# Kernel tuning notes

Measured on AMD Instinct MI355X. Metric: run time of the kernel, lower is better.

## Reference

```python
import jax, jax.numpy as jnp
import numpy as np

T, B, H, N = 1024, 8, 8, 32  # x dim D = H*N*N = 8192


def setup_inputs() -> dict:
    key = jax.random.key(0)
    x = jax.random.normal(key, (T, B, H * N * N), dtype=jnp.float32)
    S = jnp.zeros((B, H, N, N), dtype=jnp.float32)
    scale = jnp.float32(1.0)  # init_scale
    bias = jnp.float32(2.0)   # init_bias
    return {"x": x, "S": S, "scale": scale, "bias": bias}


def reference(x, S, scale, bias):
    Tt, Bb, D = x.shape
    _, Hh, n, _ = S.shape
    xr = x.reshape(Tt, Bb, Hh, n, n)  # [T,B,H,n,n]

    def step(S_c, A):
        # A: [B,H,n,n]
        k = A.mean(axis=-1)            # mean over dim 2 per head -> [B,H,n]
        v = A.mean(axis=-2)            # mean over dim 1 per head -> [B,H,n]
        A_mean = A.mean(axis=(-1, -2))  # [B,H]
        beta = jax.nn.sigmoid(scale * A_mean + bias)  # [B,H]
        k_norm = k / (jnp.linalg.norm(k, axis=-1, keepdims=True) + 1e-6)
        retrieved = jnp.einsum('bhij,bhj->bhi', S_c, k_norm)
        delta = v - retrieved
        outer = delta[..., :, None] * k_norm[..., None, :]  # [B,H,n,n]
        S_new = jnp.tanh(beta[..., None, None] * S_c + outer)
        Sq = jnp.einsum('bhij,bhj->bhi', S_new, k_norm)     # [B,H,n]
        out = Sq * jax.nn.silu(Sq)                          # [B,H,n]
        return S_new, out.reshape(Bb, Hh * n)

    S_final, output = jax.lax.scan(step, S, xr)  # output: [T,B,H*n]
    return output, S_final
```

## Files before the change

kernel.cpp:

```cpp
#include <hip/hip_runtime.h>
#include <math.h>

#define T_STEPS 1024
#define NBH     64
#define NTILE   65536
#define NCHAIN  2048
#define UNROLL  8

static __device__ __forceinline__ float fast_rcp(float x) {
  return __builtin_amdgcn_rcpf(x);
}
static __device__ __forceinline__ float fast_sigmoid(float x) {
  return fast_rcp(1.0f + __expf(-x));
}
static __device__ __forceinline__ float fast_tanh(float x) {
  return 1.0f - 2.0f * fast_rcp(1.0f + __expf(2.0f * x));
}

template <int CTRL>
static __device__ __forceinline__ float dpp_add(float x) {
  int y = __builtin_amdgcn_update_dpp(0, __float_as_int(x), CTRL, 0xF, 0xF, true);
  return x + __int_as_float(y);
}

static __device__ __forceinline__ float red32(float x) {
  x = dpp_add<0xB1>(x);
  x = dpp_add<0x4E>(x);
  x = dpp_add<0x141>(x);
  x = dpp_add<0x140>(x);
  int y = __builtin_amdgcn_ds_swizzle(__float_as_int(x), 0x401F);
  return x + __int_as_float(y);
}

__global__ __launch_bounds__(256) void stats_kernel(
    const float* __restrict__ x, const float* __restrict__ scale_p,
    const float* __restrict__ bias_p, float* __restrict__ knT,
    float* __restrict__ vvT, float* __restrict__ bbT) {
  const int tid = threadIdx.x;
  const int l   = tid & 63;
  const int m   = l & 7;
  const int g   = l >> 3;
  const int wid    = (blockIdx.x * blockDim.x + tid) >> 6;
  const int nwaves = (gridDim.x * blockDim.x) >> 6;
  const float sc = scale_p[0], bi = bias_p[0];

  for (int tile = wid; tile < NTILE; tile += nwaves) {
    const int t  = tile >> 6;
    const int bh = tile & 63;
    const float4* xp = (const float4*)(x + (size_t)tile * 1024);
    const float4 a0 = xp[l];
    const float4 a1 = xp[l + 64];
    const float4 a2 = xp[l + 128];
    const float4 a3 = xp[l + 192];

    float r0 = (a0.x + a0.y) + (a0.z + a0.w);
    float r1 = (a1.x + a1.y) + (a1.z + a1.w);
    float r2 = (a2.x + a2.y) + (a2.z + a2.w);
    float r3 = (a3.x + a3.y) + (a3.z + a3.w);
    r0 += __shfl_xor(r0, 1); r1 += __shfl_xor(r1, 1);
    r2 += __shfl_xor(r2, 1); r3 += __shfl_xor(r3, 1);
    r0 += __shfl_xor(r0, 2); r1 += __shfl_xor(r1, 2);
    r2 += __shfl_xor(r2, 2); r3 += __shfl_xor(r3, 2);
    r0 += __shfl_xor(r0, 4); r1 += __shfl_xor(r1, 4);
    r2 += __shfl_xor(r2, 4); r3 += __shfl_xor(r3, 4);

    float c0 = a0.x + a1.x + a2.x + a3.x;
    float c1 = a0.y + a1.y + a2.y + a3.y;
    float c2 = a0.z + a1.z + a2.z + a3.z;
    float c3 = a0.w + a1.w + a2.w + a3.w;
    c0 += __shfl_xor(c0, 8);  c1 += __shfl_xor(c1, 8);
    c2 += __shfl_xor(c2, 8);  c3 += __shfl_xor(c3, 8);
    c0 += __shfl_xor(c0, 16); c1 += __shfl_xor(c1, 16);
    c2 += __shfl_xor(c2, 16); c3 += __shfl_xor(c3, 16);
    c0 += __shfl_xor(c0, 32); c1 += __shfl_xor(c1, 32);
    c2 += __shfl_xor(c2, 32); c3 += __shfl_xor(c3, 32);

    float t1 = (r0 + r1) + (r2 + r3);
    float t2 = (r0 * r0 + r1 * r1) + (r2 * r2 + r3 * r3);
    t1 += __shfl_xor(t1, 8);  t2 += __shfl_xor(t2, 8);
    t1 += __shfl_xor(t1, 16); t2 += __shfl_xor(t2, 16);
    t1 += __shfl_xor(t1, 32); t2 += __shfl_xor(t2, 32);
    const float sumk  = t1 * (1.0f / 32.0f);
    const float norm  = sqrtf(t2) * (1.0f / 32.0f);
    const float ks    = (1.0f / 32.0f) * fast_rcp(norm + 1e-6f);

    const size_t rec = ((size_t)bh * T_STEPS + t) * 32;
    if (m == 0) {
      float* kp = knT + rec + g;
      kp[0]  = r0 * ks;
      kp[8]  = r1 * ks;
      kp[16] = r2 * ks;
      kp[24] = r3 * ks;
    }
    if (l < 8) {
      float4 vq;
      vq.x = c0 * (1.0f / 32.0f); vq.y = c1 * (1.0f / 32.0f);
      vq.z = c2 * (1.0f / 32.0f); vq.w = c3 * (1.0f / 32.0f);
      ((float4*)(vvT + rec))[m] = vq;
    }
    if (l == 0) {
      const float mean = sumk * (1.0f / 32.0f);
      bbT[(size_t)bh * T_STEPS + t] = fast_sigmoid(sc * mean + bi);
    }
  }
}

__global__ __launch_bounds__(256) void scan_kernel(
    const float* __restrict__ S0, const float* __restrict__ knT,
    const float* __restrict__ vvT, const float* __restrict__ bbT,
    float* __restrict__ out, float* __restrict__ Sfin) {
  const int tid   = threadIdx.x;
  const int chain = blockIdx.x * 8 + (tid >> 5);
  const int j     = tid & 31;
  const int bh    = chain >> 5;
  const int i     = chain & 31;

  float S = S0[(size_t)bh * 1024 + i * 32 + j];

  const float* knp = knT + (size_t)bh * T_STEPS * 32 + j;
  const float* vvp = vvT + (size_t)bh * T_STEPS * 32 + i;
  const float* bbp = bbT + (size_t)bh * T_STEPS;

  float rkn[UNROLL], rv[UNROLL], rb[UNROLL];
#pragma unroll
  for (int u = 0; u < UNROLL; ++u) {
    rkn[u] = knp[u * 32];
    rv[u]  = vvp[u * 32];
    rb[u]  = bbp[u];
  }

  float* outp = out + chain;

  for (int t0 = 0; t0 < T_STEPS; t0 += UNROLL) {
    float nkn[UNROLL], nv[UNROLL], nb[UNROLL];
#pragma unroll
    for (int u = 0; u < UNROLL; ++u) {
      int tn = t0 + UNROLL + u;
      tn = tn < T_STEPS ? tn : (T_STEPS - 1);
      nkn[u] = knp[(size_t)tn * 32];
      nv[u]  = vvp[(size_t)tn * 32];
      nb[u]  = bbp[tn];
    }
#pragma unroll
    for (int u = 0; u < UNROLL; ++u) {
      const float knc = rkn[u], vc = rv[u], bc = rb[u];
      const float r = red32(S * knc);
      S = fast_tanh(bc * S + (vc - r) * knc);
      const float q  = red32(S * knc);
      const float o  = q * q * fast_sigmoid(q);
      if (j == 0) outp[(size_t)(t0 + u) * 2048] = o;
    }
#pragma unroll
    for (int u = 0; u < UNROLL; ++u) {
      rkn[u] = nkn[u]; rv[u] = nv[u]; rb[u] = nb[u];
    }
  }

  Sfin[(size_t)bh * 1024 + i * 32 + j] = S;
}

extern "C" void kernel_launch(void* const* d_in, const int* in_sizes, int n_in,
                              void* d_out, int out_size, void* d_ws, size_t ws_size,
                              hipStream_t stream) {
  const float* x     = (const float*)d_in[0];
  const float* S0    = (const float*)d_in[1];
  const float* scale = (const float*)d_in[2];
  const float* bias  = (const float*)d_in[3];
  float* out = (float*)d_out;

  float* knT = (float*)d_ws;
  float* vvT = knT + (size_t)NTILE * 32;
  float* bbT = vvT + (size_t)NTILE * 32;

  stats_kernel<<<2048, 256, 0, stream>>>(x, scale, bias, knT, vvT, bbT);

  float* Sfin = out + (size_t)T_STEPS * 2048;
  scan_kernel<<<NCHAIN / 8, 256, 0, stream>>>(S0, knT, vvT, bbT, out, Sfin);
}
```

Before: 568.5 us.

## Pack two state columns per lane, transpose stats to time-major, batch output stores

The stats kernel now writes k_norm and v in a [bh][dim][T] layout, so the scan can load 16 consecutive timesteps with float4 loads and double-buffer them in registers. Each lane of the scan now holds two S entries, which shrinks the row reduction to 16 lanes using DPP only and drops the ds_swizzle. Output stores are gathered over 16 steps and written once per lane. The costs are scattered strided writes in the stats kernel, higher register pressure, and half as many blocks in the scan.

```diff
diff --git a/kernel.cpp b/kernel.cpp
--- a/kernel.cpp
+++ b/kernel.cpp
@@ -4,8 +4,6 @@
 #define T_STEPS 1024
 #define NBH     64
 #define NTILE   65536
-#define NCHAIN  2048
-#define UNROLL  8
 
 static __device__ __forceinline__ float fast_rcp(float x) {
   return __builtin_amdgcn_rcpf(x);
@@ -23,19 +21,18 @@
   return x + __int_as_float(y);
 }
 
-static __device__ __forceinline__ float red32(float x) {
+static __device__ __forceinline__ float red16(float x) {
   x = dpp_add<0xB1>(x);
   x = dpp_add<0x4E>(x);
   x = dpp_add<0x141>(x);
   x = dpp_add<0x140>(x);
-  int y = __builtin_amdgcn_ds_swizzle(__float_as_int(x), 0x401F);
-  return x + __int_as_float(y);
+  return x;
 }
 
 __global__ __launch_bounds__(256) void stats_kernel(
     const float* __restrict__ x, const float* __restrict__ scale_p,
-    const float* __restrict__ bias_p, float* __restrict__ knT,
-    float* __restrict__ vvT, float* __restrict__ bbT) {
+    const float* __restrict__ bias_p, float* __restrict__ knT2,
+    float* __restrict__ vvT2, float* __restrict__ bbT2) {
   const int tid = threadIdx.x;
   const int l   = tid & 63;
   const int m   = l & 7;
@@ -80,83 +77,101 @@
     t1 += __shfl_xor(t1, 8);  t2 += __shfl_xor(t2, 8);
     t1 += __shfl_xor(t1, 16); t2 += __shfl_xor(t2, 16);
     t1 += __shfl_xor(t1, 32); t2 += __shfl_xor(t2, 32);
-    const float sumk  = t1 * (1.0f / 32.0f);
-    const float norm  = sqrtf(t2) * (1.0f / 32.0f);
-    const float ks    = (1.0f / 32.0f) * fast_rcp(norm + 1e-6f);
+    const float norm = sqrtf(t2) * (1.0f / 32.0f);
+    const float ks   = (1.0f / 32.0f) * fast_rcp(norm + 1e-6f);
 
-    const size_t rec = ((size_t)bh * T_STEPS + t) * 32;
+    const size_t base = (size_t)bh * 32 * T_STEPS + t;
     if (m == 0) {
-      float* kp = knT + rec + g;
-      kp[0]  = r0 * ks;
-      kp[8]  = r1 * ks;
-      kp[16] = r2 * ks;
-      kp[24] = r3 * ks;
+      knT2[base + (size_t)(g)      * T_STEPS] = r0 * ks;
+      knT2[base + (size_t)(g + 8)  * T_STEPS] = r1 * ks;
+      knT2[base + (size_t)(g + 16) * T_STEPS] = r2 * ks;
+      knT2[base + (size_t)(g + 24) * T_STEPS] = r3 * ks;
     }
     if (l < 8) {
-      float4 vq;
-      vq.x = c0 * (1.0f / 32.0f); vq.y = c1 * (1.0f / 32.0f);
-      vq.z = c2 * (1.0f / 32.0f); vq.w = c3 * (1.0f / 32.0f);
-      ((float4*)(vvT + rec))[m] = vq;
+      vvT2[base + (size_t)(4 * m)     * T_STEPS] = c0 * (1.0f / 32.0f);
+      vvT2[base + (size_t)(4 * m + 1) * T_STEPS] = c1 * (1.0f / 32.0f);
+      vvT2[base + (size_t)(4 * m + 2) * T_STEPS] = c2 * (1.0f / 32.0f);
+      vvT2[base + (size_t)(4 * m + 3) * T_STEPS] = c3 * (1.0f / 32.0f);
     }
     if (l == 0) {
-      const float mean = sumk * (1.0f / 32.0f);
-      bbT[(size_t)bh * T_STEPS + t] = fast_sigmoid(sc * mean + bi);
+      const float mean = t1 * (1.0f / 1024.0f);
+      bbT2[(size_t)bh * T_STEPS + t] = fast_sigmoid(sc * mean + bi);
     }
   }
 }
 
-__global__ __launch_bounds__(256) void scan_kernel(
-    const float* __restrict__ S0, const float* __restrict__ knT,
-    const float* __restrict__ vvT, const float* __restrict__ bbT,
+__global__ __launch_bounds__(256, 1) void scan_kernel(
+    const float* __restrict__ S0, const float* __restrict__ knT2,
+    const float* __restrict__ vvT2, const float* __restrict__ bbT2,
     float* __restrict__ out, float* __restrict__ Sfin) {
-  const int tid   = threadIdx.x;
-  const int chain = blockIdx.x * 8 + (tid >> 5);
-  const int j     = tid & 31;
-  const int bh    = chain >> 5;
-  const int i     = chain & 31;
+  const int tid  = threadIdx.x;
+  const int lane = tid & 63;
+  const int g    = lane >> 4;
+  const int s    = lane & 15;
+  const int w    = blockIdx.x * 4 + (tid >> 6);
+  const int bh   = w >> 3;
+  const int i    = (w & 7) * 4 + g;
+  const int chain = bh * 32 + i;
 
-  float S = S0[(size_t)bh * 1024 + i * 32 + j];
+  const float2 sini = *(const float2*)(S0 + (size_t)bh * 1024 + i * 32 + 2 * s);
+  float Sa = sini.x, Sb = sini.y;
 
-  const float* knp = knT + (size_t)bh * T_STEPS * 32 + j;
-  const float* vvp = vvT + (size_t)bh * T_STEPS * 32 + i;
-  const float* bbp = bbT + (size_t)bh * T_STEPS;
+  const float* kn0p = knT2 + ((size_t)bh * 32 + 2 * s) * T_STEPS;
+  const float* kn1p = kn0p + T_STEPS;
+  const float* vp   = vvT2 + ((size_t)bh * 32 + i) * T_STEPS;
+  const float* bp   = bbT2 + (size_t)bh * T_STEPS;
 
-  float rkn[UNROLL], rv[UNROLL], rb[UNROLL];
-#pragma unroll
-  for (int u = 0; u < UNROLL; ++u) {
-    rkn[u] = knp[u * 32];
-    rv[u]  = vvp[u * 32];
-    rb[u]  = bbp[u];
-  }
+  float Ak0[16], Ak1[16], Av[16], Ab[16];
+  float Bk0[16], Bk1[16], Bv[16], Bb[16];
+
+#define LOAD_BLK(K0, K1, VV, BE, TOFF)                                    \
+  do {                                                                    \
+    const int _to = (TOFF);                                               \
+    _Pragma("unroll")                                                     \
+    for (int qq = 0; qq < 4; ++qq) {                                      \
+      *(float4*)&K0[4 * qq] = *(const float4*)(kn0p + _to + 4 * qq);      \
+      *(float4*)&K1[4 * qq] = *(const float4*)(kn1p + _to + 4 * qq);      \
+      *(float4*)&VV[4 * qq] = *(const float4*)(vp   + _to + 4 * qq);      \
+      *(float4*)&BE[4 * qq] = *(const float4*)(bp   + _to + 4 * qq);      \
+    }                                                                     \
+  } while (0)
+
+#define STEP_BLK(K0, K1, VV, BE, TBASE)                                   \
+  do {                                                                    \
+    float oacc = 0.0f;                                                    \
+    _Pragma("unroll")                                                     \
+    for (int u = 0; u < 16; ++u) {                                        \
+      const float c0 = K0[u], c1 = K1[u];                                 \
+      float r = red16(Sa * c0 + Sb * c1);                                 \
+      const float d  = VV[u] - r;                                         \
+      const float bc = BE[u];                                             \
+      Sa = fast_tanh(bc * Sa + d * c0);                                   \
+      Sb = fast_tanh(bc * Sb + d * c1);                                   \
+      float qv = red16(Sa * c0 + Sb * c1);                                \
+      const float o = qv * qv * fast_sigmoid(qv);                         \
+      oacc = (u == s) ? o : oacc;                                         \
+    }                                                                     \
+    outp[(size_t)((TBASE) + s) * 2048] = oacc;                            \
+  } while (0)
 
   float* outp = out + chain;
 
-  for (int t0 = 0; t0 < T_STEPS; t0 += UNROLL) {
-    float nkn[UNROLL], nv[UNROLL], nb[UNROLL];
-#pragma unroll
-    for (int u = 0; u < UNROLL; ++u) {
-      int tn = t0 + UNROLL + u;
-      tn = tn < T_STEPS ? tn : (T_STEPS - 1);
-      nkn[u] = knp[(size_t)tn * 32];
-      nv[u]  = vvp[(size_t)tn * 32];
-      nb[u]  = bbp[tn];
-    }
-#pragma unroll
-    for (int u = 0; u < UNROLL; ++u) {
-      const float knc = rkn[u], vc = rv[u], bc = rb[u];
-      const float r = red32(S * knc);
-      S = fast_tanh(bc * S + (vc - r) * knc);
-      const float q  = red32(S * knc);
-      const float o  = q * q * fast_sigmoid(q);
-      if (j == 0) outp[(size_t)(t0 + u) * 2048] = o;
-    }
-#pragma unroll
-    for (int u = 0; u < UNROLL; ++u) {
-      rkn[u] = nkn[u]; rv[u] = nv[u]; rb[u] = nb[u];
-    }
+  LOAD_BLK(Ak0, Ak1, Av, Ab, 0);
+
+  for (int t0 = 0; t0 < T_STEPS; t0 += 32) {
+    const int tB = t0 + 16;
+    const int tA2 = (t0 + 32 < T_STEPS) ? t0 + 32 : t0;
+    LOAD_BLK(Bk0, Bk1, Bv, Bb, tB);
+    STEP_BLK(Ak0, Ak1, Av, Ab, t0);
+    LOAD_BLK(Ak0, Ak1, Av, Ab, tA2);
+    STEP_BLK(Bk0, Bk1, Bv, Bb, tB);
   }
 
-  Sfin[(size_t)bh * 1024 + i * 32 + j] = S;
+#undef LOAD_BLK
+#undef STEP_BLK
+
+  float2 sfin; sfin.x = Sa; sfin.y = Sb;
+  *(float2*)(Sfin + (size_t)bh * 1024 + i * 32 + 2 * s) = sfin;
 }
 
 extern "C" void kernel_launch(void* const* d_in, const int* in_sizes, int n_in,
@@ -168,12 +183,12 @@
   const float* bias  = (const float*)d_in[3];
   float* out = (float*)d_out;
 
-  float* knT = (float*)d_ws;
-  float* vvT = knT + (size_t)NTILE * 32;
-  float* bbT = vvT + (size_t)NTILE * 32;
+  float* knT2 = (float*)d_ws;
+  float* vvT2 = knT2 + (size_t)NTILE * 32;
+  float* bbT2 = vvT2 + (size_t)NTILE * 32;
 
-  stats_kernel<<<2048, 256, 0, stream>>>(x, scale, bias, knT, vvT, bbT);
+  stats_kernel<<<2048, 256, 0, stream>>>(x, scale, bias, knT2, vvT2, bbT2);
 
   float* Sfin = out + (size_t)T_STEPS * 2048;
-  scan_kernel<<<NCHAIN / 8, 256, 0, stream>>>(S0, knT, vvT, bbT, out, Sfin);
+  scan_kernel<<<128, 256, 0, stream>>>(S0, knT2, vvT2, bbT2, out, Sfin);
 }
```

New measurement: 493.7 us. -13.2%, faster.
